# Kernel tuning notes

Measured on AMD Instinct MI355X. Metric: run time of the kernel, lower is better.

Reference implementation:

```python
import jax, jax.numpy as jnp
import numpy as np

M_FEATS = 1536      # number of proposals (docstring: [M, K])
K_DIM = 128         # feature dim per docstring example
NUM_CLASSES = 16    # label vocabulary; torch.unique loop becomes a fixed class sweep


def setup_inputs() -> dict:
    key = jax.random.key(0)
    k1, k2 = jax.random.split(key)
    features = jax.random.normal(k1, (M_FEATS, K_DIM), dtype=jnp.float32)
    labels = jax.random.randint(k2, (M_FEATS,), 0, NUM_CLASSES, dtype=jnp.int32)
    # ious all ones -> keep = (ious >= 0.5) is all-True, so the boolean filter is identity
    ious = jnp.ones((M_FEATS,), dtype=jnp.float32)
    return {"features": features, "labels": labels, "ious": ious}


def reference(features, labels, ious):
    # reweight_func='none' -> coef = ones_like(ious); keep mask is all-True by construction
    coef = jnp.ones_like(ious)
    # similarity [M, M]; coef broadcasts over columns, matching `similarity * coef` in torch
    sim = jnp.matmul(features, features.T) * coef[None, :]
    m = sim.shape[0]
    eye = jnp.eye(m, dtype=sim.dtype)
    # ground set term: logdet(similarity + 0.5 I)  (mask_ground is all ones)
    ground = jnp.linalg.slogdet(sim + 0.5 * eye)[1]

    # Per-label logdet of the submatrix S_c + 0.5 I_{n_c}. Instead of extracting a
    # variable-size submatrix (not jit-able), embed it in a full [M, M] matrix that is
    # block-diagonal: class block = S_c + 0.5 I, off-class diagonal = 1. Its logdet
    # equals logdet(S_c + 0.5 I). Absent classes give identity -> logdet 0, matching
    # torch.unique skipping them.
    onehot = (labels[:, None] == jnp.arange(NUM_CLASSES, dtype=labels.dtype)[None, :])
    onehot = onehot.astype(sim.dtype)  # [M, C]

    def class_logdet(mask):  # mask: [M] 0/1 indicator for one class
        A = sim * (mask[:, None] * mask[None, :]) + jnp.diag(0.5 * mask + (1.0 - mask))
        return jnp.linalg.slogdet(A)[1]

    per_class = jax.vmap(class_logdet)(onehot.T)  # [C]
    loss = jnp.sum(per_class) - ground
    return loss  # scalar; .mean() of a scalar is itself
```

## Files before the change

kernel.cpp:

```cpp
#include <hip/hip_runtime.h>
#include <math.h>


#define M_FEATS 1536
#define K_DIM 128
#define NUM_CLASSES 16
#define SLICE 96
#define GRAM_ELEMS (K_DIM * K_DIM)
#define PIDX(i) ((i) + ((i) >> 4))
#define SENT 0x13579BDF

__device__ __forceinline__ float chol128(
    float A[8][8], const int t, const int rg, const int cg,
    const int i0, const int j0,
    float4* panLo, float4* panHi, float4* wshLo, float4* wshHi, float* logp)
{
    if (rg == 0) {
#pragma unroll
        for (int q = 0; q < 8; ++q) {
            panLo[PIDX(j0 + q)] = make_float4(A[0][q], A[1][q], A[2][q], A[3][q]);
            panHi[PIDX(j0 + q)] = make_float4(A[4][q], A[5][q], A[6][q], A[7][q]);
        }
    }

#pragma unroll 1
    for (int s = 0; s < 16; ++s) {
        const int k = 8 * s;
        __syncthreads();

        if (t < K_DIM) {
            float4 dL[8], dH[8];
#pragma unroll
            for (int c = 0; c < 8; ++c) {
                dL[c] = panLo[PIDX(k + c)];
                dH[c] = panHi[PIDX(k + c)];
            }
            float4 aL = panLo[PIDX(t)], aH = panHi[PIDX(t)];

            float D[8][8];
#pragma unroll
            for (int c = 0; c < 8; ++c) {
                D[0][c] = dL[c].x; D[1][c] = dL[c].y;
                D[2][c] = dL[c].z; D[3][c] = dL[c].w;
                D[4][c] = dH[c].x; D[5][c] = dH[c].y;
                D[6][c] = dH[c].z; D[7][c] = dH[c].w;
            }

            float L[8][8], ic[8];
            float prod = 1.0f;
#pragma unroll
            for (int c = 0; c < 8; ++c) {
                float v = D[c][c];
#pragma unroll
                for (int m = 0; m < c; ++m) v = fmaf(-L[c][m], L[c][m], v);
                prod *= v;
                ic[c] = rsqrtf(v);
#pragma unroll
                for (int r = c + 1; r < 8; ++r) {
                    float x = D[r][c];
#pragma unroll
                    for (int m = 0; m < c; ++m) x = fmaf(-L[r][m], L[c][m], x);
                    L[r][c] = x * ic[c];
                }
            }
            if (t == 0) logp[s] = prod;

            float a[8] = {aL.x, aL.y, aL.z, aL.w, aH.x, aH.y, aH.z, aH.w};
            float w[8];
#pragma unroll
            for (int c = 0; c < 8; ++c) {
                float x = a[c];
#pragma unroll
                for (int m = 0; m < c; ++m) x = fmaf(-L[c][m], w[m], x);
                w[c] = x * ic[c];
            }
            wshLo[PIDX(t)] = make_float4(w[0], w[1], w[2], w[3]);
            wshHi[PIDX(t)] = make_float4(w[4], w[5], w[6], w[7]);
        }
        __syncthreads();

        if (rg > s && cg > s) {
            float4 wrL[8], wrH[8];
#pragma unroll
            for (int r = 0; r < 8; ++r) {
                wrL[r] = wshLo[PIDX(i0 + r)];
                wrH[r] = wshHi[PIDX(i0 + r)];
            }
#pragma unroll
            for (int q = 0; q < 8; ++q) {
                float4 wjL = wshLo[PIDX(j0 + q)];
                float4 wjH = wshHi[PIDX(j0 + q)];
#pragma unroll
                for (int r = 0; r < 8; ++r) {
                    float x = A[r][q];
                    x = fmaf(-wrL[r].x, wjL.x, x);
                    x = fmaf(-wrL[r].y, wjL.y, x);
                    x = fmaf(-wrL[r].z, wjL.z, x);
                    x = fmaf(-wrL[r].w, wjL.w, x);
                    x = fmaf(-wrH[r].x, wjH.x, x);
                    x = fmaf(-wrH[r].y, wjH.y, x);
                    x = fmaf(-wrH[r].z, wjH.z, x);
                    x = fmaf(-wrH[r].w, wjH.w, x);
                    A[r][q] = x;
                }
            }
        }
        if (rg == s + 1) {
#pragma unroll
            for (int q = 0; q < 8; ++q) {
                panLo[PIDX(j0 + q)] = make_float4(A[0][q], A[1][q], A[2][q], A[3][q]);
                panHi[PIDX(j0 + q)] = make_float4(A[4][q], A[5][q], A[6][q], A[7][q]);
            }
        }
    }

    float ls = 0.0f;
    if (t == 0) {
#pragma unroll
        for (int s = 0; s < 16; ++s) ls += logf(logp[s]);
    }
    return ls;
}

__global__ __launch_bounds__(256, 1) void fused_kernel(
    const float* __restrict__ f, const int* __restrict__ labels,
    float* __restrict__ partials, float* __restrict__ groundG,
    int* __restrict__ flag1, int* __restrict__ flag2,
    float* __restrict__ ldet, int* __restrict__ flag3,
    float* __restrict__ out)
{
    __shared__ int cnt;
    __shared__ int list[M_FEATS];
    __shared__ float4 panLo[136], panHi[136], wshLo[136], wshHi[136];
    __shared__ float logp[16];

    const int b = blockIdx.x;
    const int t = threadIdx.x;
    const int rg = t >> 4;
    const int cg = t & 15;
    const int i0 = rg << 3;
    const int j0 = cg << 3;

    float A[8][8];

    if (b < NUM_CLASSES) {
#pragma unroll
        for (int r = 0; r < 8; ++r)
#pragma unroll
            for (int q = 0; q < 8; ++q) A[r][q] = 0.0f;

        const float* base = f + (size_t)(SLICE * b) * K_DIM;
        float4 A0[6], A1[6], B0[6], B1[6];
#pragma unroll
        for (int u = 0; u < 6; ++u) {
            const float* rp = base + (size_t)u * K_DIM;
            A0[u] = *(const float4*)(rp + i0);
            A1[u] = *(const float4*)(rp + i0 + 4);
            B0[u] = *(const float4*)(rp + j0);
            B1[u] = *(const float4*)(rp + j0 + 4);
        }
        for (int jb = 0; jb < SLICE; jb += 6) {
#pragma unroll
            for (int u = 0; u < 6; ++u) {
                float fa[8] = {A0[u].x, A0[u].y, A0[u].z, A0[u].w,
                               A1[u].x, A1[u].y, A1[u].z, A1[u].w};
                float fb[8] = {B0[u].x, B0[u].y, B0[u].z, B0[u].w,
                               B1[u].x, B1[u].y, B1[u].z, B1[u].w};
#pragma unroll
                for (int r = 0; r < 8; ++r)
#pragma unroll
                    for (int q = 0; q < 8; ++q)
                        A[r][q] = fmaf(fa[r], fb[q], A[r][q]);
                int p = jb + u + 6;
                const float* rp = base + (size_t)(p < SLICE ? p : SLICE - 1) * K_DIM;
                A0[u] = *(const float4*)(rp + i0);
                A1[u] = *(const float4*)(rp + i0 + 4);
                B0[u] = *(const float4*)(rp + j0);
                B1[u] = *(const float4*)(rp + j0 + 4);
            }
        }

        float* g = partials + (size_t)b * GRAM_ELEMS;
#pragma unroll
        for (int r = 0; r < 8; ++r) {
            *(float4*)(g + (i0 + r) * K_DIM + j0) =
                make_float4(A[r][0], A[r][1], A[r][2], A[r][3]);
            *(float4*)(g + (i0 + r) * K_DIM + j0 + 4) =
                make_float4(A[r][4], A[r][5], A[r][6], A[r][7]);
        }
        __syncthreads();
        if (t == 0)
            __hip_atomic_store(&flag1[b], SENT, __ATOMIC_RELEASE,
                               __HIP_MEMORY_SCOPE_AGENT);

        if (t < NUM_CLASSES)
            while (__hip_atomic_load(&flag1[t], __ATOMIC_ACQUIRE,
                                     __HIP_MEMORY_SCOPE_AGENT) != SENT)
                __builtin_amdgcn_s_sleep(2);
        __syncthreads();

        {
            const int row = 8 * b + (t >> 5);
            const int col = (t & 31) << 2;
            float4 s = make_float4(0.f, 0.f, 0.f, 0.f);
#pragma unroll
            for (int c = 0; c < NUM_CLASSES; ++c) {
                float4 v = *(const float4*)(partials + (size_t)c * GRAM_ELEMS
                                            + row * K_DIM + col);
                s.x += v.x; s.y += v.y; s.z += v.z; s.w += v.w;
            }
            *(float4*)(groundG + row * K_DIM + col) = s;
        }
        __syncthreads();
        if (t == 0)
            __hip_atomic_store(&flag2[b], SENT, __ATOMIC_RELEASE,
                               __HIP_MEMORY_SCOPE_AGENT);
        return;
    }

    if (b < 2 * NUM_CLASSES) {
        const int cls = b - NUM_CLASSES;
        if (t == 0) cnt = 0;
        __syncthreads();
        for (int i = t; i < M_FEATS; i += 256)
            if (labels[i] == cls) list[atomicAdd(&cnt, 1)] = i;
        __syncthreads();
        const int n = cnt;

#pragma unroll
        for (int r = 0; r < 8; ++r)
#pragma unroll
            for (int q = 0; q < 8; ++q) A[r][q] = 0.0f;

        if (n > 0) {
            float4 A0[6], A1[6], B0[6], B1[6];
            int lidx[6];
#pragma unroll
            for (int u = 0; u < 6; ++u) {
                const float* rp = f + (size_t)list[u < n ? u : n - 1] * K_DIM;
                A0[u] = *(const float4*)(rp + i0);
                A1[u] = *(const float4*)(rp + i0 + 4);
                B0[u] = *(const float4*)(rp + j0);
                B1[u] = *(const float4*)(rp + j0 + 4);
                const int p = u + 6;
                lidx[u] = list[p < n ? p : n - 1];
            }
            for (int jb = 0; jb < n; jb += 6) {
#pragma unroll
                for (int u = 0; u < 6; ++u) {
                    if (jb + u < n) {
                        float fa[8] = {A0[u].x, A0[u].y, A0[u].z, A0[u].w,
                                       A1[u].x, A1[u].y, A1[u].z, A1[u].w};
                        float fb[8] = {B0[u].x, B0[u].y, B0[u].z, B0[u].w,
                                       B1[u].x, B1[u].y, B1[u].z, B1[u].w};
#pragma unroll
                        for (int r = 0; r < 8; ++r)
#pragma unroll
                            for (int q = 0; q < 8; ++q)
                                A[r][q] = fmaf(fa[r], fb[q], A[r][q]);
                    }
                    const float* rp = f + (size_t)lidx[u] * K_DIM;
                    A0[u] = *(const float4*)(rp + i0);
                    A1[u] = *(const float4*)(rp + i0 + 4);
                    B0[u] = *(const float4*)(rp + j0);
                    B1[u] = *(const float4*)(rp + j0 + 4);
                    const int p = jb + u + 12;
                    lidx[u] = list[p < n ? p : n - 1];
                }
            }
        }

#pragma unroll
        for (int r = 0; r < 8; ++r)
#pragma unroll
            for (int q = 0; q < 8; ++q)
                if ((i0 + r) == (j0 + q)) A[r][q] += 0.5f;

        float ls = chol128(A, t, rg, cg, i0, j0, panLo, panHi, wshLo, wshHi, logp);

        if (t == 0) {
            ldet[cls] = ls;
            __hip_atomic_store(&flag3[cls], SENT, __ATOMIC_RELEASE,
                               __HIP_MEMORY_SCOPE_AGENT);
        }
        return;
    }

    if (t < NUM_CLASSES)
        while (__hip_atomic_load(&flag2[t], __ATOMIC_ACQUIRE,
                                 __HIP_MEMORY_SCOPE_AGENT) != SENT)
            __builtin_amdgcn_s_sleep(2);
    __syncthreads();

#pragma unroll
    for (int r = 0; r < 8; ++r) {
        float4 v0 = *(const float4*)(groundG + (i0 + r) * K_DIM + j0);
        float4 v1 = *(const float4*)(groundG + (i0 + r) * K_DIM + j0 + 4);
        A[r][0] = v0.x; A[r][1] = v0.y; A[r][2] = v0.z; A[r][3] = v0.w;
        A[r][4] = v1.x; A[r][5] = v1.y; A[r][6] = v1.z; A[r][7] = v1.w;
    }
#pragma unroll
    for (int r = 0; r < 8; ++r)
#pragma unroll
        for (int q = 0; q < 8; ++q)
            if ((i0 + r) == (j0 + q)) A[r][q] += 0.5f;

    float ls = chol128(A, t, rg, cg, i0, j0, panLo, panHi, wshLo, wshHi, logp);

    if (t < NUM_CLASSES)
        while (__hip_atomic_load(&flag3[t], __ATOMIC_ACQUIRE,
                                 __HIP_MEMORY_SCOPE_AGENT) != SENT)
            __builtin_amdgcn_s_sleep(2);
    __syncthreads();

    if (t == 0) {
        float total = 1920.0f * 0.6931471805599453f - ls;
#pragma unroll
        for (int c = 0; c < NUM_CLASSES; ++c) total += ldet[c];
        out[0] = total;
    }
}

extern "C" void kernel_launch(void* const* d_in, const int* in_sizes, int n_in,
                              void* d_out, int out_size, void* d_ws, size_t ws_size,
                              hipStream_t stream)
{
    const float* features = (const float*)d_in[0];
    const int* labels = (const int*)d_in[1];

    float* partials = (float*)d_ws;
    float* groundG  = partials + (size_t)NUM_CLASSES * GRAM_ELEMS;
    int* flag1      = (int*)(groundG + GRAM_ELEMS);
    int* flag2      = flag1 + NUM_CLASSES;
    float* ldetp    = (float*)(flag2 + NUM_CLASSES);
    int* flag3      = (int*)(ldetp + NUM_CLASSES);

    fused_kernel<<<2 * NUM_CLASSES + 1, 256, 0, stream>>>(
        features, labels, partials, groundG, flag1, flag2, ldetp, flag3,
        (float*)d_out);
}
```

Before: 103.1 us.

## Replace per-step block barriers in Cholesky with LDS counters and double buffers

Each step of the blocked 128x128 Cholesky used to hit two __syncthreads. These are replaced by workgroup-scope atomic counters in LDS (panel-ready, w-count, update-count) that waves spin on. The panel and w buffers are double-buffered so the next panel can be published while other waves are still updating. This lets waves pipeline across steps instead of waiting on full-block barriers. The cost is spin-wait polling with s_sleep, extra LDS, and subtle ordering logic that could race or deadlock if the counts are wrong.

```diff
diff --git a/kernel.cpp b/kernel.cpp
--- a/kernel.cpp
+++ b/kernel.cpp
@@ -10,25 +10,47 @@
 #define PIDX(i) ((i) + ((i) >> 4))
 #define SENT 0x13579BDF
 
+__device__ __forceinline__ int lds_acq(int* p) {
+    return __hip_atomic_load(p, __ATOMIC_ACQUIRE, __HIP_MEMORY_SCOPE_WORKGROUP);
+}
+
 __device__ __forceinline__ float chol128(
     float A[8][8], const int t, const int rg, const int cg,
     const int i0, const int j0,
-    float4* panLo, float4* panHi, float4* wshLo, float4* wshHi, float* logp)
+    float4* panLoB, float4* panHiB, float4* wshLoB, float4* wshHiB,
+    float* logp, int* panReady, int* wshCnt, int* updCnt)
 {
+    const int wave = t >> 6;
+    const int lane0 = ((t & 63) == 0);
+
+    if (t == 0) {
+        __hip_atomic_store(panReady, 0, __ATOMIC_RELAXED, __HIP_MEMORY_SCOPE_WORKGROUP);
+        __hip_atomic_store(wshCnt, 0, __ATOMIC_RELAXED, __HIP_MEMORY_SCOPE_WORKGROUP);
+        __hip_atomic_store(updCnt, 0, __ATOMIC_RELAXED, __HIP_MEMORY_SCOPE_WORKGROUP);
+    }
+    __syncthreads();
     if (rg == 0) {
 #pragma unroll
         for (int q = 0; q < 8; ++q) {
-            panLo[PIDX(j0 + q)] = make_float4(A[0][q], A[1][q], A[2][q], A[3][q]);
-            panHi[PIDX(j0 + q)] = make_float4(A[4][q], A[5][q], A[6][q], A[7][q]);
-        }
-    }
+            panLoB[PIDX(j0 + q)] = make_float4(A[0][q], A[1][q], A[2][q], A[3][q]);
+            panHiB[PIDX(j0 + q)] = make_float4(A[4][q], A[5][q], A[6][q], A[7][q]);
+        }
+    }
+    __syncthreads();
 
 #pragma unroll 1
     for (int s = 0; s < 16; ++s) {
         const int k = 8 * s;
-        __syncthreads();
+        float4* panLo = panLoB + (s & 1) * 136;
+        float4* panHi = panHiB + (s & 1) * 136;
+        float4* wshLo = wshLoB + (s & 1) * 136;
+        float4* wshHi = wshHiB + (s & 1) * 136;
 
         if (t < K_DIM) {
+            while (lds_acq(panReady) < s) __builtin_amdgcn_s_sleep(1);
+            if (s >= 2)
+                while (lds_acq(updCnt) < 4 * (s - 1)) __builtin_amdgcn_s_sleep(1);
+
             float4 dL[8], dH[8];
 #pragma unroll
             for (int c = 0; c < 8; ++c) {
@@ -76,8 +98,12 @@
             }
             wshLo[PIDX(t)] = make_float4(w[0], w[1], w[2], w[3]);
             wshHi[PIDX(t)] = make_float4(w[4], w[5], w[6], w[7]);
-        }
-        __syncthreads();
+            if (lane0)
+                __hip_atomic_fetch_add(wshCnt, 1, __ATOMIC_RELEASE,
+                                       __HIP_MEMORY_SCOPE_WORKGROUP);
+        }
+
+        while (lds_acq(wshCnt) < 2 * (s + 1)) __builtin_amdgcn_s_sleep(1);
 
         if (rg > s && cg > s) {
             float4 wrL[8], wrH[8];
@@ -105,13 +131,21 @@
                 }
             }
         }
-        if (rg == s + 1) {
+        if (s < 15 && rg == s + 1) {
+            float4* npLo = panLoB + ((s + 1) & 1) * 136;
+            float4* npHi = panHiB + ((s + 1) & 1) * 136;
 #pragma unroll
             for (int q = 0; q < 8; ++q) {
-                panLo[PIDX(j0 + q)] = make_float4(A[0][q], A[1][q], A[2][q], A[3][q]);
-                panHi[PIDX(j0 + q)] = make_float4(A[4][q], A[5][q], A[6][q], A[7][q]);
-            }
-        }
+                npLo[PIDX(j0 + q)] = make_float4(A[0][q], A[1][q], A[2][q], A[3][q]);
+                npHi[PIDX(j0 + q)] = make_float4(A[4][q], A[5][q], A[6][q], A[7][q]);
+            }
+        }
+        if (lane0)
+            __hip_atomic_fetch_add(updCnt, 1, __ATOMIC_RELEASE,
+                                   __HIP_MEMORY_SCOPE_WORKGROUP);
+        if (s < 15 && wave == ((s + 1) >> 2) && lane0)
+            __hip_atomic_store(panReady, s + 1, __ATOMIC_RELEASE,
+                               __HIP_MEMORY_SCOPE_WORKGROUP);
     }
 
     float ls = 0.0f;
@@ -131,8 +165,9 @@
 {
     __shared__ int cnt;
     __shared__ int list[M_FEATS];
-    __shared__ float4 panLo[136], panHi[136], wshLo[136], wshHi[136];
+    __shared__ float4 panLoB[272], panHiB[272], wshLoB[272], wshHiB[272];
     __shared__ float logp[16];
+    __shared__ int panReady, wshCnt, updCnt;
 
     const int b = blockIdx.x;
     const int t = threadIdx.x;
@@ -276,7 +311,8 @@
             for (int q = 0; q < 8; ++q)
                 if ((i0 + r) == (j0 + q)) A[r][q] += 0.5f;
 
-        float ls = chol128(A, t, rg, cg, i0, j0, panLo, panHi, wshLo, wshHi, logp);
+        float ls = chol128(A, t, rg, cg, i0, j0, panLoB, panHiB, wshLoB, wshHiB,
+                           logp, &panReady, &wshCnt, &updCnt);
 
         if (t == 0) {
             ldet[cls] = ls;
@@ -305,7 +341,8 @@
         for (int q = 0; q < 8; ++q)
             if ((i0 + r) == (j0 + q)) A[r][q] += 0.5f;
 
-    float ls = chol128(A, t, rg, cg, i0, j0, panLo, panHi, wshLo, wshHi, logp);
+    float ls = chol128(A, t, rg, cg, i0, j0, panLoB, panHiB, wshLoB, wshHiB,
+                       logp, &panReady, &wshCnt, &updCnt);
 
     if (t < NUM_CLASSES)
         while (__hip_atomic_load(&flag3[t], __ATOMIC_ACQUIRE,
```

Result: slower. 106.3 us (+3.2%).
